# Performance work log

Hardware: AMD Instinct MI355X
Metric: run time of the kernel (lower is better)

## Reference

```python
import jax, jax.numpy as jnp
import numpy as np
import math

B, S, D, H = 2, 2048, 2048, 16
DH = D // H  # 128


def _rope(x, cos, sin):
    # x: [b, s, h, dh]; cos/sin: [s, dh//2]
    b, s, h, dh = x.shape
    x2 = x.reshape(b, s, h, dh // 2, 2)
    a, bb = x2[..., 0], x2[..., 1]
    c = cos[None, :, None, :]
    sn = sin[None, :, None, :]
    out = jnp.stack([a * c - bb * sn, a * sn + bb * c], axis=-1)
    return out.reshape(b, s, h, dh)


def setup_inputs() -> dict:
    key = jax.random.key(0)
    ks = jax.random.split(key, 6)
    x = jax.random.normal(ks[0], (B, S, D), dtype=jnp.float32)
    # RoPE frequencies (theta=10000) as cos/sin of shape [S, DH//2]
    inv_freq = 1.0 / (10000.0 ** (np.arange(0, DH, 2, dtype=np.float32) / DH))
    t = np.arange(S, dtype=np.float32)
    ang = jnp.asarray(np.outer(t, inv_freq))  # [S, DH//2]
    freqs_cos = jnp.cos(ang)
    freqs_sin = jnp.sin(ang)
    # causal additive mask [1,1,S,S]
    neg = jnp.finfo(jnp.float32).min
    mask = jnp.where(jnp.tril(jnp.ones((S, S), dtype=bool)), 0.0, neg)[None, None]
    sc = 0.02
    wq = jax.random.normal(ks[1], (D, D), dtype=jnp.float32) * sc
    wk = jax.random.normal(ks[2], (D, D), dtype=jnp.float32) * sc
    wv = jax.random.normal(ks[3], (D, D), dtype=jnp.float32) * sc
    wo = jax.random.normal(ks[4], (D, D), dtype=jnp.float32) * sc
    return {"x": x, "freqs_cos": freqs_cos, "freqs_sin": freqs_sin,
            "mask": mask, "wq": wq, "wk": wk, "wv": wv, "wo": wo}


def reference(x, freqs_cos, freqs_sin, mask, wq, wk, wv, wo):
    b, s, _ = x.shape
    # torch Linear: y = x @ W.T (weights stored [out, in])
    xq = (x @ wq.T).reshape(b, s, H, DH)
    xk = (x @ wk.T).reshape(b, s, H, DH)
    xv = (x @ wv.T).reshape(b, s, H, DH)
    xq = _rope(xq, freqs_cos, freqs_sin)
    xk = _rope(xk, freqs_cos, freqs_sin)
    # [b, h, s, dh]
    q = xq.transpose(0, 2, 1, 3)
    k = xk.transpose(0, 2, 1, 3)
    v = xv.transpose(0, 2, 1, 3)
    scores = jnp.einsum('bhqd,bhkd->bhqk', q, k) / math.sqrt(DH)
    scores = scores + mask
    attn = jax.nn.softmax(scores, axis=-1)  # dropout p=0 (eval)
    out = jnp.einsum('bhqk,bhkd->bhqd', attn, v)
    out = out.transpose(0, 2, 1, 3).reshape(b, s, D)
    return out @ wo.T
```

## Files before the change

kernel.cpp:

```cpp
#include <hip/hip_runtime.h>

#define B_ 2
#define S_ 2048
#define D_ 2048
#define H_ 16
#define DH_ 128

typedef __bf16 bf16_8 __attribute__((ext_vector_type(8)));
typedef __bf16 bf16_4 __attribute__((ext_vector_type(4)));
typedef float f32x4 __attribute__((ext_vector_type(4)));

__device__ __forceinline__ f32x4 mfma16(bf16_8 a, bf16_8 b, f32x4 c) {
  return __builtin_amdgcn_mfma_f32_16x16x32_bf16(a, b, c, 0, 0, 0);
}

__device__ __forceinline__ bf16_8 load8(const float* p) {
  f32x4 a = *(const f32x4*)p;
  f32x4 b = *(const f32x4*)(p + 4);
  bf16_8 r;
  r[0] = (__bf16)a[0]; r[1] = (__bf16)a[1]; r[2] = (__bf16)a[2]; r[3] = (__bf16)a[3];
  r[4] = (__bf16)b[0]; r[5] = (__bf16)b[1]; r[6] = (__bf16)b[2]; r[7] = (__bf16)b[3];
  return r;
}

__device__ __forceinline__ void async16(const __bf16* g, __bf16* l) {
  __builtin_amdgcn_global_load_lds(
      (const __attribute__((address_space(1))) void*)g,
      (__attribute__((address_space(3))) void*)l, 16, 0, 0);
}

__global__ __launch_bounds__(256) void cvt_all(
    const float* __restrict__ x, const float* __restrict__ wq,
    const float* __restrict__ wk, const float* __restrict__ wv,
    const float* __restrict__ wo, __bf16* __restrict__ xb,
    __bf16* __restrict__ wqb, __bf16* __restrict__ wkb,
    __bf16* __restrict__ wvb, __bf16* __restrict__ wob)
{
  const int W8 = (D_ * D_) / 8;
  int i = blockIdx.x * 256 + threadIdx.x;
  if (i < 2 * W8) {
    *(bf16_8*)(xb + (size_t)i * 8) = load8(x + (size_t)i * 8);
  } else {
    int j = i - 2 * W8;
    int sel = j >> 19, off = j & (W8 - 1);
    const float* s = sel == 0 ? wq : sel == 1 ? wk : sel == 2 ? wv : wo;
    __bf16* d = sel == 0 ? wqb : sel == 1 ? wkb : sel == 2 ? wvb : wob;
    *(bf16_8*)(d + (size_t)off * 8) = load8(s + (size_t)off * 8);
  }
}

template <bool WB>
__global__ __launch_bounds__(256) void qkv_gemm(
    const __bf16* __restrict__ A,
    const float* __restrict__ wqf, const float* __restrict__ wkf,
    const float* __restrict__ wvf,
    const __bf16* __restrict__ wqb, const __bf16* __restrict__ wkb,
    const __bf16* __restrict__ wvb,
    const float* __restrict__ fc, const float* __restrict__ fs,
    __bf16* __restrict__ Qo, __bf16* __restrict__ Ko, __bf16* __restrict__ Vo)
{
  __shared__ __bf16 As[128][32];
  __shared__ __bf16 Ws[128][WB ? 32 : 40];
  const int tid = threadIdx.x;
  const int wave = tid >> 6, lane = tid & 63;
  const int quad = lane >> 4, l16 = lane & 15;
  const int m0 = blockIdx.y * 128, n0 = blockIdx.x * 128;
  const int wsel = n0 >> 11, nloc = n0 & 2047;
  const int wm = (wave >> 1) * 64, wn = (wave & 1) * 64;
  const __bf16* agl = A + (size_t)(m0 + wave * 32 + (lane >> 2)) * 2048 + (lane & 3) * 8;
  f32x4 acc[4][4] = {};
  if (WB) {
    const __bf16* Wb = wsel == 0 ? wqb : wsel == 1 ? wkb : wvb;
    const __bf16* wgl = Wb + (size_t)(nloc + wave * 32 + (lane >> 2)) * 2048 + (lane & 3) * 8;
    for (int k0 = 0; k0 < 2048; k0 += 32) {
      __syncthreads();
      async16(agl + k0,             &As[wave * 32][0]);
      async16(agl + 16 * 2048 + k0, &As[wave * 32 + 16][0]);
      async16(wgl + k0,             &Ws[wave * 32][0]);
      async16(wgl + 16 * 2048 + k0, &Ws[wave * 32 + 16][0]);
      __syncthreads();
      bf16_8 af[4], bfr[4];
      for (int i = 0; i < 4; ++i) {
        af[i]  = *(const bf16_8*)&As[wm + i * 16 + l16][quad * 8];
        bfr[i] = *(const bf16_8*)&Ws[wn + i * 16 + l16][quad * 8];
      }
      for (int mi = 0; mi < 4; ++mi)
        for (int ni = 0; ni < 4; ++ni)
          acc[mi][ni] = mfma16(af[mi], bfr[ni], acc[mi][ni]);
    }
  } else {
    const float* W = wsel == 0 ? wqf : wsel == 1 ? wkf : wvf;
    const int srow = tid >> 1, scol = (tid & 1) * 16;
    const float* wg = W + (size_t)(nloc + srow) * 2048 + scol;
    for (int k0 = 0; k0 < 2048; k0 += 32) {
      __syncthreads();
      async16(agl + k0,             &As[wave * 32][0]);
      async16(agl + 16 * 2048 + k0, &As[wave * 32 + 16][0]);
      *(bf16_8*)&Ws[srow][scol]     = load8(wg + k0);
      *(bf16_8*)&Ws[srow][scol + 8] = load8(wg + k0 + 8);
      __syncthreads();
      bf16_8 af[4], bfr[4];
      for (int i = 0; i < 4; ++i) {
        af[i]  = *(const bf16_8*)&As[wm + i * 16 + l16][quad * 8];
        bfr[i] = *(const bf16_8*)&Ws[wn + i * 16 + l16][quad * 8];
      }
      for (int mi = 0; mi < 4; ++mi)
        for (int ni = 0; ni < 4; ++ni)
          acc[mi][ni] = mfma16(af[mi], bfr[ni], acc[mi][ni]);
    }
  }
  if (wsel < 2) {
    const float qscale = wsel == 0 ? 0.08838834764831845f * 1.4426950408889634f
                                   : 1.0f;
    __bf16* O = wsel == 0 ? Qo : Ko;
    for (int mi = 0; mi < 4; ++mi)
      for (int ni = 0; ni < 4; ++ni)
        for (int r = 0; r < 4; ++r) {
          int row = m0 + wm + mi * 16 + quad * 4 + r;
          int col = nloc + wn + ni * 16 + l16;
          float self = acc[mi][ni][r];
          float oth = __shfl_xor(self, 1);
          int s = row & (S_ - 1);
          int dh = col & (DH_ - 1);
          float c = fc[s * (DH_ / 2) + (dh >> 1)];
          float sn = fs[s * (DH_ / 2) + (dh >> 1)];
          float o = (dh & 1) ? (oth * sn + self * c) : (self * c - oth * sn);
          O[(size_t)row * 2048 + col] = (__bf16)(o * qscale);
        }
  } else {
    for (int mi = 0; mi < 4; ++mi)
      for (int ni = 0; ni < 4; ++ni) {
        int col = nloc + wn + ni * 16 + l16;
        int row0 = m0 + wm + mi * 16 + quad * 4;
        int b = row0 >> 11, s = row0 & (S_ - 1);
        int h = col >> 7, dh = col & (DH_ - 1);
        bf16_4 pk;
        for (int r = 0; r < 4; ++r) pk[r] = (__bf16)acc[mi][ni][r];
        *(bf16_4*)(Vo + ((size_t)(b * H_ + h) * DH_ + dh) * S_ + s) = pk;
      }
  }
}

template <bool WB>
__global__ __launch_bounds__(256) void out_gemm(
    const __bf16* __restrict__ A, const float* __restrict__ Wf,
    const __bf16* __restrict__ Wb, float* __restrict__ C)
{
  __shared__ __bf16 As[128][32];
  __shared__ __bf16 Ws[128][WB ? 32 : 40];
  const int tid = threadIdx.x;
  const int wave = tid >> 6, lane = tid & 63;
  const int quad = lane >> 4, l16 = lane & 15;
  const int m0 = blockIdx.y * 128, n0 = blockIdx.x * 128;
  const int wm = (wave >> 1) * 64, wn = (wave & 1) * 64;
  const __bf16* agl = A + (size_t)(m0 + wave * 32 + (lane >> 2)) * 2048 + (lane & 3) * 8;
  f32x4 acc[4][4] = {};
  if (WB) {
    const __bf16* wgl = Wb + (size_t)(n0 + wave * 32 + (lane >> 2)) * 2048 + (lane & 3) * 8;
    for (int k0 = 0; k0 < 2048; k0 += 32) {
      __syncthreads();
      async16(agl + k0,             &As[wave * 32][0]);
      async16(agl + 16 * 2048 + k0, &As[wave * 32 + 16][0]);
      async16(wgl + k0,             &Ws[wave * 32][0]);
      async16(wgl + 16 * 2048 + k0, &Ws[wave * 32 + 16][0]);
      __syncthreads();
      bf16_8 af[4], bfr[4];
      for (int i = 0; i < 4; ++i) {
        af[i]  = *(const bf16_8*)&As[wm + i * 16 + l16][quad * 8];
        bfr[i] = *(const bf16_8*)&Ws[wn + i * 16 + l16][quad * 8];
      }
      for (int mi = 0; mi < 4; ++mi)
        for (int ni = 0; ni < 4; ++ni)
          acc[mi][ni] = mfma16(af[mi], bfr[ni], acc[mi][ni]);
    }
  } else {
    const int srow = tid >> 1, scol = (tid & 1) * 16;
    const float* wg = Wf + (size_t)(n0 + srow) * 2048 + scol;
    for (int k0 = 0; k0 < 2048; k0 += 32) {
      __syncthreads();
      async16(agl + k0,             &As[wave * 32][0]);
      async16(agl + 16 * 2048 + k0, &As[wave * 32 + 16][0]);
      *(bf16_8*)&Ws[srow][scol]     = load8(wg + k0);
      *(bf16_8*)&Ws[srow][scol + 8] = load8(wg + k0 + 8);
      __syncthreads();
      bf16_8 af[4], bfr[4];
      for (int i = 0; i < 4; ++i) {
        af[i]  = *(const bf16_8*)&As[wm + i * 16 + l16][quad * 8];
        bfr[i] = *(const bf16_8*)&Ws[wn + i * 16 + l16][quad * 8];
      }
      for (int mi = 0; mi < 4; ++mi)
        for (int ni = 0; ni < 4; ++ni)
          acc[mi][ni] = mfma16(af[mi], bfr[ni], acc[mi][ni]);
    }
  }
  for (int mi = 0; mi < 4; ++mi)
    for (int ni = 0; ni < 4; ++ni)
      for (int r = 0; r < 4; ++r) {
        int row = m0 + wm + mi * 16 + quad * 4 + r;
        int col = n0 + wn + ni * 16 + l16;
        C[(size_t)row * 2048 + col] = acc[mi][ni][r];
      }
}

__global__ __launch_bounds__(256) void attn_kernel(
    const __bf16* __restrict__ Q, const __bf16* __restrict__ K,
    const __bf16* __restrict__ Vt_g, __bf16* __restrict__ O)
{
  __shared__ __bf16 Ks[64][136];
  __shared__ __bf16 Vt[128][72];
  __shared__ __bf16 Ps[4][16][72];
  const int tid = threadIdx.x;
  const int wave = tid >> 6, lane = tid & 63;
  const int quad = lane >> 4, l16 = lane & 15;
  const int bh = blockIdx.y;
  const int b = bh >> 4, h = bh & 15;
  const size_t base = (size_t)b * S_ * D_ + (size_t)h * DH_;
  const size_t vtb = (size_t)bh * DH_ * S_;
  const int kr = tid >> 4, kc = (tid & 15) * 8;
  const int vr = tid >> 3, vc = (tid & 7) * 8;
  const int NT = S_ / 64;

  for (int ph = 0; ph < 2; ++ph) {
    const int qt = ph ? (int)blockIdx.x : (NT - 1 - (int)blockIdx.x);
    const int q0 = qt * 64;
    const int qrow = q0 + wave * 16 + l16;
    bf16_8 qf[4];
    for (int kk = 0; kk < 4; ++kk)
      qf[kk] = *(const bf16_8*)(Q + base + (size_t)qrow * D_ + kk * 32 + quad * 8);
    f32x4 oacc[8] = {};
    float lsum[4] = {};
    for (int kt = 0; kt <= qt; ++kt) {
      __syncthreads();
      for (int p = 0; p < 4; ++p) {
        int krl = p * 16 + kr;
        *(bf16_8*)&Ks[krl][kc] =
            *(const bf16_8*)(K + base + (size_t)(kt * 64 + krl) * D_ + kc);
      }
      for (int p = 0; p < 4; ++p) {
        int dh = p * 32 + vr;
        *(bf16_8*)&Vt[dh][vc] =
            *(const bf16_8*)(Vt_g + vtb + (size_t)dh * S_ + kt * 64 + vc);
      }
      __syncthreads();
      float sc[4][4];
      for (int n = 0; n < 4; ++n) {
        f32x4 sacc = {};
        for (int kk = 0; kk < 4; ++kk) {
          bf16_8 kf = *(const bf16_8*)&Ks[n * 16 + l16][kk * 32 + quad * 8];
          sacc = mfma16(qf[kk], kf, sacc);
        }
        for (int r = 0; r < 4; ++r) sc[n][r] = sacc[r];
      }
      if (kt == qt) {
        for (int r = 0; r < 4; ++r) {
          int qr = wave * 16 + quad * 4 + r;
          for (int n = 0; n < 4; ++n)
            if (n * 16 + l16 > qr) sc[n][r] = -INFINITY;
        }
      }
      for (int r = 0; r < 4; ++r)
        for (int n = 0; n < 4; ++n) {
          float p = exp2f(sc[n][r]);
          lsum[r] += p;
          Ps[wave][quad * 4 + r][n * 16 + l16] = (__bf16)p;
        }
      bf16_8 pf0 = *(const bf16_8*)&Ps[wave][l16][quad * 8];
      bf16_8 pf1 = *(const bf16_8*)&Ps[wave][l16][32 + quad * 8];
      for (int nc = 0; nc < 8; ++nc) {
        bf16_8 vf0 = *(const bf16_8*)&Vt[nc * 16 + l16][quad * 8];
        bf16_8 vf1 = *(const bf16_8*)&Vt[nc * 16 + l16][32 + quad * 8];
        oacc[nc] = mfma16(pf0, vf0, oacc[nc]);
        oacc[nc] = mfma16(pf1, vf1, oacc[nc]);
      }
    }
    for (int r = 0; r < 4; ++r) {
      float l = lsum[r];
      l += __shfl_xor(l, 1);
      l += __shfl_xor(l, 2);
      l += __shfl_xor(l, 4);
      l += __shfl_xor(l, 8);
      float rinv = 1.f / l;
      int qr = q0 + wave * 16 + quad * 4 + r;
      for (int nc = 0; nc < 8; ++nc)
        O[base + (size_t)qr * D_ + nc * 16 + l16] = (__bf16)(oacc[nc][r] * rinv);
    }
  }
}

extern "C" void kernel_launch(void* const* d_in, const int* in_sizes, int n_in,
                              void* d_out, int out_size, void* d_ws, size_t ws_size,
                              hipStream_t stream)
{
  const float* x    = (const float*)d_in[0];
  const float* fcos = (const float*)d_in[1];
  const float* fsin = (const float*)d_in[2];
  const float* wq   = (const float*)d_in[4];
  const float* wk   = (const float*)d_in[5];
  const float* wv   = (const float*)d_in[6];
  const float* wo   = (const float*)d_in[7];
  float* out = (float*)d_out;

  const size_t T = (size_t)B_ * S_ * D_;
  const size_t W = (size_t)D_ * D_;
  __bf16* xb  = (__bf16*)d_ws;
  __bf16* qw  = xb + T;
  __bf16* kw  = qw + T;
  __bf16* vt  = kw + T;
  __bf16* wqb = vt + T;
  __bf16* wkb = wqb + W;
  __bf16* wvb = wkb + W;
  __bf16* wob = wvb + W;
  __bf16* ow  = xb;

  const bool wb = ws_size >= (4 * T + 4 * W) * sizeof(__bf16);
  const int W8 = (int)(W / 8);
  cvt_all<<<(wb ? 6 : 2) * W8 / 256, 256, 0, stream>>>(
      x, wq, wk, wv, wo, xb, wqb, wkb, wvb, wob);
  if (wb)
    qkv_gemm<true><<<dim3(48, 32), 256, 0, stream>>>(
        xb, nullptr, nullptr, nullptr, wqb, wkb, wvb, fcos, fsin, qw, kw, vt);
  else
    qkv_gemm<false><<<dim3(48, 32), 256, 0, stream>>>(
        xb, wq, wk, wv, nullptr, nullptr, nullptr, fcos, fsin, qw, kw, vt);
  attn_kernel<<<dim3(S_ / 128, B_ * H_), 256, 0, stream>>>(qw, kw, vt, ow);
  if (wb)
    out_gemm<true><<<dim3(16, 32), 256, 0, stream>>>(ow, nullptr, wob, out);
  else
    out_gemm<false><<<dim3(16, 32), 256, 0, stream>>>(ow, wo, nullptr, out);
}
```

Baseline: 474.0 us.

## Read K/V fragments directly from global memory and launch one block per query tile

The attention kernel no longer stages K and V tiles in shared memory with block-wide barriers. Each wave now loads its MFMA operand fragments straight from global memory and relies on cache for reuse across the four waves. The grid is doubled to one query tile per block instead of a paired heavy/light tile loop, trading causal load balancing for more blocks. The aim is to remove barriers and LDS traffic, at the risk of redundant, poorly coalesced global loads and load imbalance across blocks.

```diff
diff --git a/kernel.cpp b/kernel.cpp
--- a/kernel.cpp
+++ b/kernel.cpp
@@ -206,84 +206,77 @@
     const __bf16* __restrict__ Q, const __bf16* __restrict__ K,
     const __bf16* __restrict__ Vt_g, __bf16* __restrict__ O)
 {
-  __shared__ __bf16 Ks[64][136];
-  __shared__ __bf16 Vt[128][72];
   __shared__ __bf16 Ps[4][16][72];
   const int tid = threadIdx.x;
   const int wave = tid >> 6, lane = tid & 63;
   const int quad = lane >> 4, l16 = lane & 15;
+  const int qt = gridDim.x - 1 - blockIdx.x;
   const int bh = blockIdx.y;
   const int b = bh >> 4, h = bh & 15;
   const size_t base = (size_t)b * S_ * D_ + (size_t)h * DH_;
   const size_t vtb = (size_t)bh * DH_ * S_;
-  const int kr = tid >> 4, kc = (tid & 15) * 8;
-  const int vr = tid >> 3, vc = (tid & 7) * 8;
-  const int NT = S_ / 64;
-
-  for (int ph = 0; ph < 2; ++ph) {
-    const int qt = ph ? (int)blockIdx.x : (NT - 1 - (int)blockIdx.x);
-    const int q0 = qt * 64;
-    const int qrow = q0 + wave * 16 + l16;
-    bf16_8 qf[4];
-    for (int kk = 0; kk < 4; ++kk)
-      qf[kk] = *(const bf16_8*)(Q + base + (size_t)qrow * D_ + kk * 32 + quad * 8);
-    f32x4 oacc[8] = {};
-    float lsum[4] = {};
-    for (int kt = 0; kt <= qt; ++kt) {
-      __syncthreads();
-      for (int p = 0; p < 4; ++p) {
-        int krl = p * 16 + kr;
-        *(bf16_8*)&Ks[krl][kc] =
-            *(const bf16_8*)(K + base + (size_t)(kt * 64 + krl) * D_ + kc);
-      }
-      for (int p = 0; p < 4; ++p) {
-        int dh = p * 32 + vr;
-        *(bf16_8*)&Vt[dh][vc] =
-            *(const bf16_8*)(Vt_g + vtb + (size_t)dh * S_ + kt * 64 + vc);
-      }
-      __syncthreads();
-      float sc[4][4];
+  const int q0 = qt * 64;
+
+  const int qrow = q0 + wave * 16 + l16;
+  bf16_8 qf[4];
+  for (int kk = 0; kk < 4; ++kk)
+    qf[kk] = *(const bf16_8*)(Q + base + (size_t)qrow * D_ + kk * 32 + quad * 8);
+
+  f32x4 oacc[8] = {};
+  float lsum[4] = {};
+
+  const __bf16* kfb = K + base + (size_t)l16 * D_ + quad * 8;
+  const __bf16* vfb = Vt_g + vtb + (size_t)l16 * S_ + quad * 8;
+
+  for (int kt = 0; kt <= qt; ++kt) {
+    const __bf16* kp = kfb + (size_t)(kt * 64) * D_;
+    float sc[4][4];
+#pragma unroll
+    for (int n = 0; n < 4; ++n) {
+      f32x4 sacc = {};
+#pragma unroll
+      for (int kk = 0; kk < 4; ++kk) {
+        bf16_8 kf = *(const bf16_8*)(kp + (size_t)(n * 16) * D_ + kk * 32);
+        sacc = mfma16(qf[kk], kf, sacc);
+      }
+      for (int r = 0; r < 4; ++r) sc[n][r] = sacc[r];
+    }
+    if (kt == qt) {
+      for (int r = 0; r < 4; ++r) {
+        int qr = wave * 16 + quad * 4 + r;
+        for (int n = 0; n < 4; ++n)
+          if (n * 16 + l16 > qr) sc[n][r] = -INFINITY;
+      }
+    }
+#pragma unroll
+    for (int r = 0; r < 4; ++r)
       for (int n = 0; n < 4; ++n) {
-        f32x4 sacc = {};
-        for (int kk = 0; kk < 4; ++kk) {
-          bf16_8 kf = *(const bf16_8*)&Ks[n * 16 + l16][kk * 32 + quad * 8];
-          sacc = mfma16(qf[kk], kf, sacc);
-        }
-        for (int r = 0; r < 4; ++r) sc[n][r] = sacc[r];
-      }
-      if (kt == qt) {
-        for (int r = 0; r < 4; ++r) {
-          int qr = wave * 16 + quad * 4 + r;
-          for (int n = 0; n < 4; ++n)
-            if (n * 16 + l16 > qr) sc[n][r] = -INFINITY;
-        }
-      }
-      for (int r = 0; r < 4; ++r)
-        for (int n = 0; n < 4; ++n) {
-          float p = exp2f(sc[n][r]);
-          lsum[r] += p;
-          Ps[wave][quad * 4 + r][n * 16 + l16] = (__bf16)p;
-        }
-      bf16_8 pf0 = *(const bf16_8*)&Ps[wave][l16][quad * 8];
-      bf16_8 pf1 = *(const bf16_8*)&Ps[wave][l16][32 + quad * 8];
-      for (int nc = 0; nc < 8; ++nc) {
-        bf16_8 vf0 = *(const bf16_8*)&Vt[nc * 16 + l16][quad * 8];
-        bf16_8 vf1 = *(const bf16_8*)&Vt[nc * 16 + l16][32 + quad * 8];
-        oacc[nc] = mfma16(pf0, vf0, oacc[nc]);
-        oacc[nc] = mfma16(pf1, vf1, oacc[nc]);
-      }
-    }
-    for (int r = 0; r < 4; ++r) {
-      float l = lsum[r];
-      l += __shfl_xor(l, 1);
-      l += __shfl_xor(l, 2);
-      l += __shfl_xor(l, 4);
-      l += __shfl_xor(l, 8);
-      float rinv = 1.f / l;
-      int qr = q0 + wave * 16 + quad * 4 + r;
-      for (int nc = 0; nc < 8; ++nc)
-        O[base + (size_t)qr * D_ + nc * 16 + l16] = (__bf16)(oacc[nc][r] * rinv);
-    }
+        float p = exp2f(sc[n][r]);
+        lsum[r] += p;
+        Ps[wave][quad * 4 + r][n * 16 + l16] = (__bf16)p;
+      }
+    bf16_8 pf0 = *(const bf16_8*)&Ps[wave][l16][quad * 8];
+    bf16_8 pf1 = *(const bf16_8*)&Ps[wave][l16][32 + quad * 8];
+    const __bf16* vp = vfb + kt * 64;
+#pragma unroll
+    for (int nc = 0; nc < 8; ++nc) {
+      bf16_8 vf0 = *(const bf16_8*)(vp + (size_t)(nc * 16) * S_);
+      bf16_8 vf1 = *(const bf16_8*)(vp + (size_t)(nc * 16) * S_ + 32);
+      oacc[nc] = mfma16(pf0, vf0, oacc[nc]);
+      oacc[nc] = mfma16(pf1, vf1, oacc[nc]);
+    }
+  }
+
+  for (int r = 0; r < 4; ++r) {
+    float l = lsum[r];
+    l += __shfl_xor(l, 1);
+    l += __shfl_xor(l, 2);
+    l += __shfl_xor(l, 4);
+    l += __shfl_xor(l, 8);
+    float rinv = 1.f / l;
+    int qr = q0 + wave * 16 + quad * 4 + r;
+    for (int nc = 0; nc < 8; ++nc)
+      O[base + (size_t)qr * D_ + nc * 16 + l16] = (__bf16)(oacc[nc][r] * rinv);
   }
 }
 
@@ -322,7 +315,7 @@
   else
     qkv_gemm<false><<<dim3(48, 32), 256, 0, stream>>>(
         xb, wq, wk, wv, nullptr, nullptr, nullptr, fcos, fsin, qw, kw, vt);
-  attn_kernel<<<dim3(S_ / 128, B_ * H_), 256, 0, stream>>>(qw, kw, vt, ow);
+  attn_kernel<<<dim3(S_ / 64, B_ * H_), 256, 0, stream>>>(qw, kw, vt, ow);
   if (wb)
     out_gemm<true><<<dim3(16, 32), 256, 0, stream>>>(ow, nullptr, wob, out);
   else
```

Result: slower. 788.3 us (+66.3%).
